# Optimization experiments

Hardware: AMD Instinct MI355X
Metric: run time of the kernel (lower is better)

## Reference

```python
import jax, jax.numpy as jnp
import numpy as np

N0, N1, N2, N3 = 100000, 200000, 150000, 50000
C = 64            # all in/intermediate/out channel widths
SLOPE = 0.2       # leaky_relu negative slope


def seg_softmax(vals, seg, n):
    """Row-wise sparse softmax (torch.sparse.softmax, dim=1) over COO values."""
    m = jax.ops.segment_max(vals, seg, num_segments=n)
    ex = jnp.exp(vals - m[seg])
    s = jax.ops.segment_sum(ex, seg, num_segments=n)
    return ex / s[seg]


def hbs(x, row, col, W, a, n):
    """HBS block (m_hop=1): att(i,j)=softmax_i(lrelu([m_i||m_j]a)); y = A_att @ m."""
    m = x @ W                                   # [n, C]
    a1, a2 = a[:C], a[C:]
    e = jax.nn.leaky_relu(m[row] @ a1 + m[col] @ a2, SLOPE)  # per-nnz logit
    att = seg_softmax(e, row, n)
    return jax.ops.segment_sum(att[:, None] * m[col], row, num_segments=n)


def hbns(xs, xt, ti, sj, Ws, Wt, a, ns, nt):
    """HBNS block. neighborhood is [nt, ns] with COO indices (ti, sj).
    Returns (message_on_source [ns,C], message_on_target [nt,C])."""
    sm = xs @ Ws                                # [ns, C] source messages
    tm = xt @ Wt                                # [nt, C] target messages
    a1, a2 = a[:C], a[C:]
    sm_j = sm[sj]
    tm_i = tm[ti]
    e = jax.nn.leaky_relu(sm_j @ a1 + tm_i @ a2, SLOPE)  # s->t logits, rows=ti
    f = jax.nn.leaky_relu(tm_i @ a1 + sm_j @ a2, SLOPE)  # t->s logits, rows=sj
    att_e = seg_softmax(e, ti, nt)
    att_f = seg_softmax(f, sj, ns)
    msg_t = jax.ops.segment_sum(att_e[:, None] * sm_j, ti, num_segments=nt)
    msg_s = jax.ops.segment_sum(att_f[:, None] * tm_i, sj, num_segments=ns)
    return msg_s, msg_t


def setup_inputs() -> dict:
    key = jax.random.key(0)
    ks = jax.random.split(key, 32)
    def randn(k, shape):
        return jax.random.normal(k, shape, dtype=jnp.float32)
    def ridx(k, n, hi):
        return jax.random.randint(k, (n,), 0, hi, dtype=jnp.int32)
    g = 0.1  # weight scale (~xavier for 64-dim)
    return dict(
        x_0=randn(ks[0], (N0, C)), x_1=randn(ks[1], (N1, C)),
        x_2=randn(ks[2], (N2, C)), x_3=randn(ks[3], (N3, C)),
        # 5 HBS blocks: [0_l1, 0_l2, 1_l2, 2_l2, 3_l2]
        hbs_W=randn(ks[4], (5, C, C)) * g,
        hbs_a=randn(ks[5], (5, 2 * C)) * g,
        # 6 HBNS blocks: [01_l1, 12_l1, 23_l1, 01_l2, 12_l2, 23_l2]
        hbns_Ws=randn(ks[6], (6, C, C)) * g,
        hbns_Wt=randn(ks[7], (6, C, C)) * g,
        hbns_a=randn(ks[8], (6, 2 * C)) * g,
        adj0_row=ridx(ks[9], 1000000, N0), adj0_col=ridx(ks[10], 1000000, N0),
        adj1_row=ridx(ks[11], 1000000, N1), adj1_col=ridx(ks[12], 1000000, N1),
        adj2_row=ridx(ks[13], 800000, N2), adj2_col=ridx(ks[14], 800000, N2),
        coadj3_row=ridx(ks[15], 300000, N3), coadj3_col=ridx(ks[16], 300000, N3),
        inc1_row=ridx(ks[17], 400000, N0), inc1_col=ridx(ks[18], 400000, N1),
        inc2_row=ridx(ks[19], 450000, N1), inc2_col=ridx(ks[20], 450000, N2),
        inc3_row=ridx(ks[21], 200000, N2), inc3_col=ridx(ks[22], 200000, N3),
    )


def reference(x_0, x_1, x_2, x_3, hbs_W, hbs_a, hbns_Ws, hbns_Wt, hbns_a,
              adj0_row, adj0_col, adj1_row, adj1_col, adj2_row, adj2_col,
              coadj3_row, coadj3_col, inc1_row, inc1_col, inc2_row, inc2_col,
              inc3_row, inc3_col):
    n0, n1, n2, n3 = x_0.shape[0], x_1.shape[0], x_2.shape[0], x_3.shape[0]
    # ---- level 1 ----
    x00 = hbs(x_0, adj0_row, adj0_col, hbs_W[0], hbs_a[0], n0)
    x01, x10 = hbns(x_1, x_0, inc1_row, inc1_col, hbns_Ws[0], hbns_Wt[0], hbns_a[0], n1, n0)
    x12, x21 = hbns(x_2, x_1, inc2_row, inc2_col, hbns_Ws[1], hbns_Wt[1], hbns_a[1], n2, n1)
    x23, x32 = hbns(x_3, x_2, inc3_row, inc3_col, hbns_Ws[2], hbns_Wt[2], hbns_a[2], n3, n2)
    x0_l1 = x00 + x10
    x1_l1 = x01 + x21
    x2_l1 = x12 + x32
    x3_l1 = x23
    # ---- level 2 ----
    y00 = hbs(x0_l1, adj0_row, adj0_col, hbs_W[1], hbs_a[1], n0)
    y11 = hbs(x1_l1, adj1_row, adj1_col, hbs_W[2], hbs_a[2], n1)
    y22 = hbs(x2_l1, adj2_row, adj2_col, hbs_W[3], hbs_a[3], n2)
    y33 = hbs(x3_l1, coadj3_row, coadj3_col, hbs_W[4], hbs_a[4], n3)
    y01, _ = hbns(x1_l1, x0_l1, inc1_row, inc1_col, hbns_Ws[3], hbns_Wt[3], hbns_a[3], n1, n0)
    y12, _ = hbns(x2_l1, x1_l1, inc2_row, inc2_col, hbns_Ws[4], hbns_Wt[4], hbns_a[4], n2, n1)
    y23, _ = hbns(x3_l1, x2_l1, inc3_row, inc3_col, hbns_Ws[5], hbns_Wt[5], hbns_a[5], n3, n2)
    return (y00, y01 + y11, y12 + y22, y23 + y33)
```

## Files before the change

kernel.cpp:

```cpp
#include <hip/hip_runtime.h>
#include <cstddef>
#include <cstdint>

#define LRELU_SLOPE 0.2f
#define SCAN_BLK 256
#define SCAN_ELEMS 2048

#define XS_STRIDE 68

__global__ __launch_bounds__(256, 4) void gemm_pq_kernel(
    const float* __restrict__ x, const float* __restrict__ W,
    const float* __restrict__ a, float* __restrict__ m,
    float* __restrict__ p, float* __restrict__ q, int n)
{
    __shared__ float xs[64 * XS_STRIDE];
    __shared__ float ws[64 * XS_STRIDE];

    const int t = threadIdx.x;
    const int rbase = blockIdx.x * 64;

    {
        const float4* __restrict__ W4 = (const float4*)W;
#pragma unroll
        for (int u = 0; u < 4; ++u) {
            int f = t + 256 * u;
            int k = f >> 4, g = f & 15;
            float4 v = W4[f];
            *(float4*)&ws[k * XS_STRIDE + 4 * g] = v;
        }
    }
    {
        const float4* __restrict__ x4 = (const float4*)x;
#pragma unroll
        for (int u = 0; u < 4; ++u) {
            int f = t + 256 * u;
            int r = f >> 4, g = f & 15;
            float4 v = make_float4(0.f, 0.f, 0.f, 0.f);
            if (rbase + r < n) v = x4[(size_t)(rbase + r) * 16 + g];
            *(float4*)&xs[r * XS_STRIDE + 4 * g] = v;
        }
    }
    __syncthreads();

    const int lane = t & 63;
    const int wv   = t >> 6;
    const int s    = lane & 15;
    const int rg   = lane >> 4;
    const int c0   = 4 * s;
    const int r0   = 16 * wv + 4 * rg;

    float acc[4][4] = {{0.f}};

#pragma unroll 2
    for (int k0 = 0; k0 < 64; k0 += 4) {
        float xr[4][4], wr[4][4];
#pragma unroll
        for (int i = 0; i < 4; ++i) {
            float4 v = *(const float4*)&xs[(r0 + i) * XS_STRIDE + k0];
            xr[i][0] = v.x; xr[i][1] = v.y; xr[i][2] = v.z; xr[i][3] = v.w;
        }
#pragma unroll
        for (int kk = 0; kk < 4; ++kk) {
            float4 v = *(const float4*)&ws[(k0 + kk) * XS_STRIDE + c0];
            wr[kk][0] = v.x; wr[kk][1] = v.y; wr[kk][2] = v.z; wr[kk][3] = v.w;
        }
#pragma unroll
        for (int kk = 0; kk < 4; ++kk)
#pragma unroll
            for (int i = 0; i < 4; ++i)
#pragma unroll
                for (int j = 0; j < 4; ++j)
                    acc[i][j] = fmaf(xr[i][kk], wr[kk][j], acc[i][j]);
    }

#pragma unroll
    for (int i = 0; i < 4; ++i) {
        int r = rbase + r0 + i;
        if (r < n)
            *(float4*)&m[(size_t)r * 64 + c0] =
                make_float4(acc[i][0], acc[i][1], acc[i][2], acc[i][3]);
    }

    const float4 a1v = *(const float4*)&a[c0];
    const float4 a2v = *(const float4*)&a[64 + c0];
    float pp[4], qq[4];
#pragma unroll
    for (int i = 0; i < 4; ++i) {
        pp[i] = fmaf(acc[i][3], a1v.w, fmaf(acc[i][2], a1v.z,
                fmaf(acc[i][1], a1v.y, acc[i][0] * a1v.x)));
        qq[i] = fmaf(acc[i][3], a2v.w, fmaf(acc[i][2], a2v.z,
                fmaf(acc[i][1], a2v.y, acc[i][0] * a2v.x)));
    }
#pragma unroll
    for (int off = 1; off < 16; off <<= 1) {
#pragma unroll
        for (int i = 0; i < 4; ++i) {
            pp[i] += __shfl_xor(pp[i], off);
            qq[i] += __shfl_xor(qq[i], off);
        }
    }
    if (s == 0) {
#pragma unroll
        for (int i = 0; i < 4; ++i) {
            int r = rbase + r0 + i;
            if (r < n) { p[r] = pp[i]; q[r] = qq[i]; }
        }
    }
}

__global__ __launch_bounds__(256) void hist1(const int* __restrict__ seg,
                                             int* __restrict__ counts, int base, int E)
{
    int k = blockIdx.x * blockDim.x + threadIdx.x;
    if (k < E) atomicAdd(&counts[base + seg[k]], 1);
}

__global__ __launch_bounds__(256) void hist2(const int* __restrict__ a, const int* __restrict__ b,
                                             int* __restrict__ counts, int baseA, int baseB, int E)
{
    int k = blockIdx.x * blockDim.x + threadIdx.x;
    if (k < E) {
        atomicAdd(&counts[baseA + a[k]], 1);
        atomicAdd(&counts[baseB + b[k]], 1);
    }
}

__global__ __launch_bounds__(SCAN_BLK) void scan_partial(const int* __restrict__ in,
                                                         int* __restrict__ out,
                                                         int* __restrict__ bsums, int n)
{
    __shared__ int lds[SCAN_BLK];
    int base = blockIdx.x * SCAN_ELEMS + threadIdx.x * 8;
    int v[8]; int s = 0;
#pragma unroll
    for (int k = 0; k < 8; ++k) { int x = (base + k < n) ? in[base + k] : 0; v[k] = s; s += x; }
    lds[threadIdx.x] = s;
    __syncthreads();
    int t = s;
    for (int off = 1; off < SCAN_BLK; off <<= 1) {
        int y = (threadIdx.x >= off) ? lds[threadIdx.x - off] : 0;
        __syncthreads();
        t += y;
        lds[threadIdx.x] = t;
        __syncthreads();
    }
    int excl = t - s;
    if (threadIdx.x == SCAN_BLK - 1) bsums[blockIdx.x] = t;
#pragma unroll
    for (int k = 0; k < 8; ++k) if (base + k < n) out[base + k] = excl + v[k];
}

__global__ __launch_bounds__(1024) void scan_top(int* __restrict__ bsums, int nb)
{
    __shared__ int lds[1024];
    int x = (threadIdx.x < nb) ? bsums[threadIdx.x] : 0;
    lds[threadIdx.x] = x;
    __syncthreads();
    int t = x;
    for (int off = 1; off < 1024; off <<= 1) {
        int y = (threadIdx.x >= off) ? lds[threadIdx.x - off] : 0;
        __syncthreads();
        t += y;
        lds[threadIdx.x] = t;
        __syncthreads();
    }
    if (threadIdx.x < nb) bsums[threadIdx.x] = t - x;
}

__global__ __launch_bounds__(256) void scan_addback(int* __restrict__ out,
                                                    const int* __restrict__ bsums, int n)
{
    int i = blockIdx.x * blockDim.x + threadIdx.x;
    if (i < n) out[i] += bsums[i / SCAN_ELEMS];
}

__global__ __launch_bounds__(256) void place1(const int* __restrict__ seg, const int* __restrict__ other,
                                              const int* __restrict__ rs, int* __restrict__ counts,
                                              int* __restrict__ colsAll, int base, int E)
{
    int k = blockIdx.x * blockDim.x + threadIdx.x;
    if (k >= E) return;
    int s = base + seg[k];
    int off = atomicSub(&counts[s], 1) - 1;
    colsAll[rs[s] + off] = other[k];
}

__global__ __launch_bounds__(256) void place2(const int* __restrict__ a, const int* __restrict__ b,
                                              const int* __restrict__ rs, int* __restrict__ counts,
                                              int* __restrict__ colsAll, int baseA, int baseB, int E)
{
    int k = blockIdx.x * blockDim.x + threadIdx.x;
    if (k >= E) return;
    int av = a[k], bv = b[k];
    int sa = baseA + av;
    int offa = atomicSub(&counts[sa], 1) - 1;
    colsAll[rs[sa] + offa] = bv;
    int sb = baseB + bv;
    int offb = atomicSub(&counts[sb], 1) - 1;
    colsAll[rs[sb] + offb] = av;
}

__global__ __launch_bounds__(256) void seg_agg(
    const int* __restrict__ rs, const int* __restrict__ cols,
    const float* __restrict__ uni, const float* __restrict__ gat,
    const float* __restrict__ feat, float* __restrict__ out, int n)
{
    const int sub = threadIdx.x & 15;
    int row = (int)((blockIdx.x * blockDim.x + threadIdx.x) >> 4);
    if (row >= n) return;
    int e0 = rs[row], e1 = rs[row + 1];
    if (e0 >= e1) return;
    const float pu = uni[row];
    const float4* __restrict__ feat4 = (const float4*)feat;
    float4 acc = make_float4(0.f, 0.f, 0.f, 0.f);
    float ssum = 0.f;
    int e = e0;
    for (; e + 1 < e1; e += 2) {
        int c0 = cols[e], c1 = cols[e + 1];
        float g0 = gat[c0], g1 = gat[c1];
        float4 f0 = feat4[(size_t)c0 * 16 + sub];
        float4 f1 = feat4[(size_t)c1 * 16 + sub];
        float t0 = pu + g0; t0 = (t0 > 0.f) ? t0 : LRELU_SLOPE * t0;
        float t1 = pu + g1; t1 = (t1 > 0.f) ? t1 : LRELU_SLOPE * t1;
        float w0 = __expf(t0);
        float w1 = __expf(t1);
        ssum += w0 + w1;
        acc.x = fmaf(w0, f0.x, acc.x); acc.y = fmaf(w0, f0.y, acc.y);
        acc.z = fmaf(w0, f0.z, acc.z); acc.w = fmaf(w0, f0.w, acc.w);
        acc.x = fmaf(w1, f1.x, acc.x); acc.y = fmaf(w1, f1.y, acc.y);
        acc.z = fmaf(w1, f1.z, acc.z); acc.w = fmaf(w1, f1.w, acc.w);
    }
    if (e < e1) {
        int c0 = cols[e];
        float g0 = gat[c0];
        float4 f0 = feat4[(size_t)c0 * 16 + sub];
        float t0 = pu + g0; t0 = (t0 > 0.f) ? t0 : LRELU_SLOPE * t0;
        float w0 = __expf(t0);
        ssum += w0;
        acc.x = fmaf(w0, f0.x, acc.x); acc.y = fmaf(w0, f0.y, acc.y);
        acc.z = fmaf(w0, f0.z, acc.z); acc.w = fmaf(w0, f0.w, acc.w);
    }
    float inv = __frcp_rn(ssum);
    float4* __restrict__ out4 = (float4*)out;
    float4 o = out4[(size_t)row * 16 + sub];
    o.x = fmaf(acc.x, inv, o.x); o.y = fmaf(acc.y, inv, o.y);
    o.z = fmaf(acc.z, inv, o.z); o.w = fmaf(acc.w, inv, o.w);
    out4[(size_t)row * 16 + sub] = o;
}

extern "C" void kernel_launch(void* const* d_in, const int* in_sizes, int n_in,
                              void* d_out, int out_size, void* d_ws, size_t ws_size,
                              hipStream_t stream)
{
    const float* x0 = (const float*)d_in[0];
    const float* x1 = (const float*)d_in[1];
    const float* x2 = (const float*)d_in[2];
    const float* x3 = (const float*)d_in[3];
    const float* hbsW = (const float*)d_in[4];
    const float* hbsA = (const float*)d_in[5];
    const float* hWs  = (const float*)d_in[6];
    const float* hWt  = (const float*)d_in[7];
    const float* hA   = (const float*)d_in[8];
    const int* a0r = (const int*)d_in[9];  const int* a0c = (const int*)d_in[10];
    const int* a1r = (const int*)d_in[11]; const int* a1c = (const int*)d_in[12];
    const int* a2r = (const int*)d_in[13]; const int* a2c = (const int*)d_in[14];
    const int* c3r = (const int*)d_in[15]; const int* c3c = (const int*)d_in[16];
    const int* i1r = (const int*)d_in[17]; const int* i1c = (const int*)d_in[18];
    const int* i2r = (const int*)d_in[19]; const int* i2c = (const int*)d_in[20];
    const int* i3r = (const int*)d_in[21]; const int* i3c = (const int*)d_in[22];

    const int n0 = in_sizes[0] / 64, n1 = in_sizes[1] / 64;
    const int n2 = in_sizes[2] / 64, n3 = in_sizes[3] / 64;
    const int Ea0 = in_sizes[9],  Ea1 = in_sizes[11], Ea2 = in_sizes[13], Ec3 = in_sizes[15];
    const int Ei1 = in_sizes[17], Ei2 = in_sizes[19], Ei3 = in_sizes[21];

    int nm = n0; if (n1 > nm) nm = n1; if (n2 > nm) nm = n2; if (n3 > nm) nm = n3;

    int b_adj0 = 0;
    int b_adj1 = b_adj0 + n0;
    int b_adj2 = b_adj1 + n1;
    int b_c3   = b_adj2 + n2;
    int b_i1t  = b_c3   + n3;
    int b_i1s  = b_i1t  + n0;
    int b_i2t  = b_i1s  + n1;
    int b_i2s  = b_i2t  + n1;
    int b_i3t  = b_i2s  + n2;
    int b_i3s  = b_i3t  + n2;
    int NC     = b_i3s  + n3 + 1;
    long long eTot = (long long)Ea0 + Ea1 + Ea2 + Ec3 + 2LL * (Ei1 + Ei2 + Ei3);

    float* w = (float*)d_ws;
    size_t off = 0;
    auto allocf = [&](size_t nel) { float* r = w + off; off += nel; return r; };
    float* featA = allocf((size_t)nm * 64);
    float* featB = allocf((size_t)nm * 64);
    float* xl10  = allocf((size_t)n0 * 64);
    float* xl11  = allocf((size_t)n1 * 64);
    float* xl12  = allocf((size_t)n2 * 64);
    float* xl13  = allocf((size_t)n3 * 64);
    float* pA = allocf(nm); float* qA = allocf(nm);
    float* pB = allocf(nm); float* qB = allocf(nm);
    int* counts  = (int*)allocf((size_t)NC);
    int* rs      = (int*)allocf((size_t)NC);
    int* bsums   = (int*)allocf(1024);
    int* colsAll = (int*)allocf((size_t)eTot);

    if (off * sizeof(float) > ws_size) {
        hipMemsetAsync(d_out, 0, (size_t)out_size * sizeof(float), stream);
        return;
    }

    float* out  = (float*)d_out;
    float* out0 = out;
    float* out1 = out0 + (size_t)n0 * 64;
    float* out2 = out1 + (size_t)n1 * 64;
    float* out3 = out2 + (size_t)n2 * 64;

    hipMemsetAsync(xl10, 0, (size_t)(n0 + n1 + n2 + n3) * 64 * sizeof(float), stream);
    hipMemsetAsync(counts, 0, (size_t)NC * sizeof(int), stream);
    hipMemsetAsync(d_out, 0, (size_t)out_size * sizeof(float), stream);

    auto blks = [](int n, int per) { return dim3((unsigned)((n + per - 1) / per)); };

    hist1<<<blks(Ea0, 256), 256, 0, stream>>>(a0r, counts, b_adj0, Ea0);
    hist1<<<blks(Ea1, 256), 256, 0, stream>>>(a1r, counts, b_adj1, Ea1);
    hist1<<<blks(Ea2, 256), 256, 0, stream>>>(a2r, counts, b_adj2, Ea2);
    hist1<<<blks(Ec3, 256), 256, 0, stream>>>(c3r, counts, b_c3,  Ec3);
    hist2<<<blks(Ei1, 256), 256, 0, stream>>>(i1r, i1c, counts, b_i1t, b_i1s, Ei1);
    hist2<<<blks(Ei2, 256), 256, 0, stream>>>(i2r, i2c, counts, b_i2t, b_i2s, Ei2);
    hist2<<<blks(Ei3, 256), 256, 0, stream>>>(i3r, i3c, counts, b_i3t, b_i3s, Ei3);

    int nb = (NC + SCAN_ELEMS - 1) / SCAN_ELEMS;
    scan_partial<<<dim3((unsigned)nb), SCAN_BLK, 0, stream>>>(counts, rs, bsums, NC);
    scan_top<<<dim3(1), 1024, 0, stream>>>(bsums, nb);
    scan_addback<<<blks(NC, 256), 256, 0, stream>>>(rs, bsums, NC);

    place1<<<blks(Ea0, 256), 256, 0, stream>>>(a0r, a0c, rs, counts, colsAll, b_adj0, Ea0);
    place1<<<blks(Ea1, 256), 256, 0, stream>>>(a1r, a1c, rs, counts, colsAll, b_adj1, Ea1);
    place1<<<blks(Ea2, 256), 256, 0, stream>>>(a2r, a2c, rs, counts, colsAll, b_adj2, Ea2);
    place1<<<blks(Ec3, 256), 256, 0, stream>>>(c3r, c3c, rs, counts, colsAll, b_c3,  Ec3);
    place2<<<blks(Ei1, 256), 256, 0, stream>>>(i1r, i1c, rs, counts, colsAll, b_i1t, b_i1s, Ei1);
    place2<<<blks(Ei2, 256), 256, 0, stream>>>(i2r, i2c, rs, counts, colsAll, b_i2t, b_i2s, Ei2);
    place2<<<blks(Ei3, 256), 256, 0, stream>>>(i3r, i3c, rs, counts, colsAll, b_i3t, b_i3s, Ei3);

    auto gemm = [&](const float* xx, const float* WW, const float* aa,
                    float* mm, float* pp, float* qq, int n) {
        gemm_pq_kernel<<<blks(n, 64), 256, 0, stream>>>(xx, WW, aa, mm, pp, qq, n);
    };
    auto agg = [&](int base, const float* uni, const float* gat,
                   const float* feat, float* outp, int n) {
        seg_agg<<<blks(n, 16), 256, 0, stream>>>(rs + base, colsAll, uni, gat, feat, outp, n);
    };

    gemm(x0, hbsW + 0 * 4096, hbsA + 0 * 128, featA, pA, qA, n0);
    agg(b_adj0, pA, qA, featA, xl10, n0);

    gemm(x1, hWs + 0 * 4096, hA + 0 * 128, featA, pA, qA, n1);
    gemm(x0, hWt + 0 * 4096, hA + 0 * 128, featB, pB, qB, n0);
    agg(b_i1t, qB, pA, featA, xl10, n0);
    agg(b_i1s, qA, pB, featB, xl11, n1);

    gemm(x2, hWs + 1 * 4096, hA + 1 * 128, featA, pA, qA, n2);
    gemm(x1, hWt + 1 * 4096, hA + 1 * 128, featB, pB, qB, n1);
    agg(b_i2t, qB, pA, featA, xl11, n1);
    agg(b_i2s, qA, pB, featB, xl12, n2);

    gemm(x3, hWs + 2 * 4096, hA + 2 * 128, featA, pA, qA, n3);
    gemm(x2, hWt + 2 * 4096, hA + 2 * 128, featB, pB, qB, n2);
    agg(b_i3t, qB, pA, featA, xl12, n2);
    agg(b_i3s, qA, pB, featB, xl13, n3);

    gemm(xl10, hbsW + 1 * 4096, hbsA + 1 * 128, featA, pA, qA, n0);
    agg(b_adj0, pA, qA, featA, out0, n0);

    gemm(xl11, hbsW + 2 * 4096, hbsA + 2 * 128, featA, pA, qA, n1);
    agg(b_adj1, pA, qA, featA, out1, n1);

    gemm(xl12, hbsW + 3 * 4096, hbsA + 3 * 128, featA, pA, qA, n2);
    agg(b_adj2, pA, qA, featA, out2, n2);

    gemm(xl13, hbsW + 4 * 4096, hbsA + 4 * 128, featA, pA, qA, n3);
    agg(b_c3, pA, qA, featA, out3, n3);

    gemm(xl11, hWs + 3 * 4096, hA + 3 * 128, featA, pA, qA, n1);
    gemm(xl10, hWt + 3 * 4096, hA + 3 * 128, featB, pB, qB, n0);
    agg(b_i1s, qA, pB, featB, out1, n1);

    gemm(xl12, hWs + 4 * 4096, hA + 4 * 128, featA, pA, qA, n2);
    gemm(xl11, hWt + 4 * 4096, hA + 4 * 128, featB, pB, qB, n1);
    agg(b_i2s, qA, pB, featB, out2, n2);

    gemm(xl13, hWs + 5 * 4096, hA + 5 * 128, featA, pA, qA, n3);
    gemm(xl12, hWs != hWt ? hWt + 5 * 4096 : hWt + 5 * 4096, hA + 5 * 128, featB, pB, qB, n2);
    agg(b_i3s, qA, pB, featB, out3, n3);
}
```

Measured before the change: 1.727 ms.

## Drop output memsets via store-mode aggregation and vectorize COO histogram/placement

Adds a STORE template mode to seg_agg so the first aggregation into each buffer writes its result directly, zero-filling empty rows, instead of read-modify-writing a pre-zeroed buffer. This removes two large memsets and a read per row on first writes. The histogram and placement kernels now have each thread handle four edges through int4 loads, with the grid shrunk to match. The gain depends on every output buffer being written first by a STORE call, so a wrong call order would silently corrupt results.

```diff
diff --git a/kernel.cpp b/kernel.cpp
--- a/kernel.cpp
+++ b/kernel.cpp
@@ -111,17 +111,38 @@
 __global__ __launch_bounds__(256) void hist1(const int* __restrict__ seg,
                                              int* __restrict__ counts, int base, int E)
 {
-    int k = blockIdx.x * blockDim.x + threadIdx.x;
-    if (k < E) atomicAdd(&counts[base + seg[k]], 1);
+    int k0 = (blockIdx.x * blockDim.x + threadIdx.x) * 4;
+    if (k0 + 3 < E) {
+        int4 s4 = *(const int4*)&seg[k0];
+        atomicAdd(&counts[base + s4.x], 1);
+        atomicAdd(&counts[base + s4.y], 1);
+        atomicAdd(&counts[base + s4.z], 1);
+        atomicAdd(&counts[base + s4.w], 1);
+    } else {
+        for (int k = k0; k < E; ++k) atomicAdd(&counts[base + seg[k]], 1);
+    }
 }
 
 __global__ __launch_bounds__(256) void hist2(const int* __restrict__ a, const int* __restrict__ b,
                                              int* __restrict__ counts, int baseA, int baseB, int E)
 {
-    int k = blockIdx.x * blockDim.x + threadIdx.x;
-    if (k < E) {
-        atomicAdd(&counts[baseA + a[k]], 1);
-        atomicAdd(&counts[baseB + b[k]], 1);
+    int k0 = (blockIdx.x * blockDim.x + threadIdx.x) * 4;
+    if (k0 + 3 < E) {
+        int4 a4 = *(const int4*)&a[k0];
+        int4 b4 = *(const int4*)&b[k0];
+        atomicAdd(&counts[baseA + a4.x], 1);
+        atomicAdd(&counts[baseA + a4.y], 1);
+        atomicAdd(&counts[baseA + a4.z], 1);
+        atomicAdd(&counts[baseA + a4.w], 1);
+        atomicAdd(&counts[baseB + b4.x], 1);
+        atomicAdd(&counts[baseB + b4.y], 1);
+        atomicAdd(&counts[baseB + b4.z], 1);
+        atomicAdd(&counts[baseB + b4.w], 1);
+    } else {
+        for (int k = k0; k < E; ++k) {
+            atomicAdd(&counts[baseA + a[k]], 1);
+            atomicAdd(&counts[baseB + b[k]], 1);
+        }
     }
 }
 
@@ -178,28 +199,68 @@
                                               const int* __restrict__ rs, int* __restrict__ counts,
                                               int* __restrict__ colsAll, int base, int E)
 {
-    int k = blockIdx.x * blockDim.x + threadIdx.x;
-    if (k >= E) return;
-    int s = base + seg[k];
-    int off = atomicSub(&counts[s], 1) - 1;
-    colsAll[rs[s] + off] = other[k];
+    int k0 = (blockIdx.x * blockDim.x + threadIdx.x) * 4;
+    if (k0 + 3 < E) {
+        int4 s4 = *(const int4*)&seg[k0];
+        int4 o4 = *(const int4*)&other[k0];
+        int sa = base + s4.x, sb = base + s4.y, sc = base + s4.z, sd = base + s4.w;
+        int oa = atomicSub(&counts[sa], 1) - 1;
+        int ob = atomicSub(&counts[sb], 1) - 1;
+        int oc = atomicSub(&counts[sc], 1) - 1;
+        int od = atomicSub(&counts[sd], 1) - 1;
+        colsAll[rs[sa] + oa] = o4.x;
+        colsAll[rs[sb] + ob] = o4.y;
+        colsAll[rs[sc] + oc] = o4.z;
+        colsAll[rs[sd] + od] = o4.w;
+    } else {
+        for (int k = k0; k < E; ++k) {
+            int s = base + seg[k];
+            int off = atomicSub(&counts[s], 1) - 1;
+            colsAll[rs[s] + off] = other[k];
+        }
+    }
 }
 
 __global__ __launch_bounds__(256) void place2(const int* __restrict__ a, const int* __restrict__ b,
                                               const int* __restrict__ rs, int* __restrict__ counts,
                                               int* __restrict__ colsAll, int baseA, int baseB, int E)
 {
-    int k = blockIdx.x * blockDim.x + threadIdx.x;
-    if (k >= E) return;
-    int av = a[k], bv = b[k];
-    int sa = baseA + av;
-    int offa = atomicSub(&counts[sa], 1) - 1;
-    colsAll[rs[sa] + offa] = bv;
-    int sb = baseB + bv;
-    int offb = atomicSub(&counts[sb], 1) - 1;
-    colsAll[rs[sb] + offb] = av;
-}
-
+    int k0 = (blockIdx.x * blockDim.x + threadIdx.x) * 4;
+    if (k0 + 3 < E) {
+        int4 a4 = *(const int4*)&a[k0];
+        int4 b4 = *(const int4*)&b[k0];
+        int sa0 = baseA + a4.x, sa1 = baseA + a4.y, sa2 = baseA + a4.z, sa3 = baseA + a4.w;
+        int sb0 = baseB + b4.x, sb1 = baseB + b4.y, sb2 = baseB + b4.z, sb3 = baseB + b4.w;
+        int oa0 = atomicSub(&counts[sa0], 1) - 1;
+        int oa1 = atomicSub(&counts[sa1], 1) - 1;
+        int oa2 = atomicSub(&counts[sa2], 1) - 1;
+        int oa3 = atomicSub(&counts[sa3], 1) - 1;
+        int ob0 = atomicSub(&counts[sb0], 1) - 1;
+        int ob1 = atomicSub(&counts[sb1], 1) - 1;
+        int ob2 = atomicSub(&counts[sb2], 1) - 1;
+        int ob3 = atomicSub(&counts[sb3], 1) - 1;
+        colsAll[rs[sa0] + oa0] = b4.x;
+        colsAll[rs[sa1] + oa1] = b4.y;
+        colsAll[rs[sa2] + oa2] = b4.z;
+        colsAll[rs[sa3] + oa3] = b4.w;
+        colsAll[rs[sb0] + ob0] = a4.x;
+        colsAll[rs[sb1] + ob1] = a4.y;
+        colsAll[rs[sb2] + ob2] = a4.z;
+        colsAll[rs[sb3] + ob3] = a4.w;
+    } else {
+        for (int k = k0; k < E; ++k) {
+            int av = a[k], bv = b[k];
+            int sa = baseA + av;
+            int offa = atomicSub(&counts[sa], 1) - 1;
+            colsAll[rs[sa] + offa] = bv;
+            int sb = baseB + bv;
+            int offb = atomicSub(&counts[sb], 1) - 1;
+            colsAll[rs[sb] + offb] = av;
+        }
+    }
+}
+
+template<bool STORE>
 __global__ __launch_bounds__(256) void seg_agg(
     const int* __restrict__ rs, const int* __restrict__ cols,
     const float* __restrict__ uni, const float* __restrict__ gat,
@@ -208,8 +269,12 @@
     const int sub = threadIdx.x & 15;
     int row = (int)((blockIdx.x * blockDim.x + threadIdx.x) >> 4);
     if (row >= n) return;
+    float4* __restrict__ out4 = (float4*)out;
     int e0 = rs[row], e1 = rs[row + 1];
-    if (e0 >= e1) return;
+    if (e0 >= e1) {
+        if (STORE) out4[(size_t)row * 16 + sub] = make_float4(0.f, 0.f, 0.f, 0.f);
+        return;
+    }
     const float pu = uni[row];
     const float4* __restrict__ feat4 = (const float4*)feat;
     float4 acc = make_float4(0.f, 0.f, 0.f, 0.f);
@@ -241,11 +306,15 @@
         acc.z = fmaf(w0, f0.z, acc.z); acc.w = fmaf(w0, f0.w, acc.w);
     }
     float inv = __frcp_rn(ssum);
-    float4* __restrict__ out4 = (float4*)out;
-    float4 o = out4[(size_t)row * 16 + sub];
-    o.x = fmaf(acc.x, inv, o.x); o.y = fmaf(acc.y, inv, o.y);
-    o.z = fmaf(acc.z, inv, o.z); o.w = fmaf(acc.w, inv, o.w);
-    out4[(size_t)row * 16 + sub] = o;
+    if (STORE) {
+        out4[(size_t)row * 16 + sub] =
+            make_float4(acc.x * inv, acc.y * inv, acc.z * inv, acc.w * inv);
+    } else {
+        float4 o = out4[(size_t)row * 16 + sub];
+        o.x = fmaf(acc.x, inv, o.x); o.y = fmaf(acc.y, inv, o.y);
+        o.z = fmaf(acc.z, inv, o.z); o.w = fmaf(acc.w, inv, o.w);
+        out4[(size_t)row * 16 + sub] = o;
+    }
 }
 
 extern "C" void kernel_launch(void* const* d_in, const int* in_sizes, int n_in,
@@ -316,81 +385,83 @@
     float* out2 = out1 + (size_t)n1 * 64;
     float* out3 = out2 + (size_t)n2 * 64;
 
-    hipMemsetAsync(xl10, 0, (size_t)(n0 + n1 + n2 + n3) * 64 * sizeof(float), stream);
     hipMemsetAsync(counts, 0, (size_t)NC * sizeof(int), stream);
-    hipMemsetAsync(d_out, 0, (size_t)out_size * sizeof(float), stream);
 
     auto blks = [](int n, int per) { return dim3((unsigned)((n + per - 1) / per)); };
 
-    hist1<<<blks(Ea0, 256), 256, 0, stream>>>(a0r, counts, b_adj0, Ea0);
-    hist1<<<blks(Ea1, 256), 256, 0, stream>>>(a1r, counts, b_adj1, Ea1);
-    hist1<<<blks(Ea2, 256), 256, 0, stream>>>(a2r, counts, b_adj2, Ea2);
-    hist1<<<blks(Ec3, 256), 256, 0, stream>>>(c3r, counts, b_c3,  Ec3);
-    hist2<<<blks(Ei1, 256), 256, 0, stream>>>(i1r, i1c, counts, b_i1t, b_i1s, Ei1);
-    hist2<<<blks(Ei2, 256), 256, 0, stream>>>(i2r, i2c, counts, b_i2t, b_i2s, Ei2);
-    hist2<<<blks(Ei3, 256), 256, 0, stream>>>(i3r, i3c, counts, b_i3t, b_i3s, Ei3);
+    hist1<<<blks(Ea0, 1024), 256, 0, stream>>>(a0r, counts, b_adj0, Ea0);
+    hist1<<<blks(Ea1, 1024), 256, 0, stream>>>(a1r, counts, b_adj1, Ea1);
+    hist1<<<blks(Ea2, 1024), 256, 0, stream>>>(a2r, counts, b_adj2, Ea2);
+    hist1<<<blks(Ec3, 1024), 256, 0, stream>>>(c3r, counts, b_c3,  Ec3);
+    hist2<<<blks(Ei1, 1024), 256, 0, stream>>>(i1r, i1c, counts, b_i1t, b_i1s, Ei1);
+    hist2<<<blks(Ei2, 1024), 256, 0, stream>>>(i2r, i2c, counts, b_i2t, b_i2s, Ei2);
+    hist2<<<blks(Ei3, 1024), 256, 0, stream>>>(i3r, i3c, counts, b_i3t, b_i3s, Ei3);
 
     int nb = (NC + SCAN_ELEMS - 1) / SCAN_ELEMS;
     scan_partial<<<dim3((unsigned)nb), SCAN_BLK, 0, stream>>>(counts, rs, bsums, NC);
     scan_top<<<dim3(1), 1024, 0, stream>>>(bsums, nb);
     scan_addback<<<blks(NC, 256), 256, 0, stream>>>(rs, bsums, NC);
 
-    place1<<<blks(Ea0, 256), 256, 0, stream>>>(a0r, a0c, rs, counts, colsAll, b_adj0, Ea0);
-    place1<<<blks(Ea1, 256), 256, 0, stream>>>(a1r, a1c, rs, counts, colsAll, b_adj1, Ea1);
-    place1<<<blks(Ea2, 256), 256, 0, stream>>>(a2r, a2c, rs, counts, colsAll, b_adj2, Ea2);
-    place1<<<blks(Ec3, 256), 256, 0, stream>>>(c3r, c3c, rs, counts, colsAll, b_c3,  Ec3);
-    place2<<<blks(Ei1, 256), 256, 0, stream>>>(i1r, i1c, rs, counts, colsAll, b_i1t, b_i1s, Ei1);
-    place2<<<blks(Ei2, 256), 256, 0, stream>>>(i2r, i2c, rs, counts, colsAll, b_i2t, b_i2s, Ei2);
-    place2<<<blks(Ei3, 256), 256, 0, stream>>>(i3r, i3c, rs, counts, colsAll, b_i3t, b_i3s, Ei3);
+    place1<<<blks(Ea0, 1024), 256, 0, stream>>>(a0r, a0c, rs, counts, colsAll, b_adj0, Ea0);
+    place1<<<blks(Ea1, 1024), 256, 0, stream>>>(a1r, a1c, rs, counts, colsAll, b_adj1, Ea1);
+    place1<<<blks(Ea2, 1024), 256, 0, stream>>>(a2r, a2c, rs, counts, colsAll, b_adj2, Ea2);
+    place1<<<blks(Ec3, 1024), 256, 0, stream>>>(c3r, c3c, rs, counts, colsAll, b_c3,  Ec3);
+    place2<<<blks(Ei1, 1024), 256, 0, stream>>>(i1r, i1c, rs, counts, colsAll, b_i1t, b_i1s, Ei1);
+    place2<<<blks(Ei2, 1024), 256, 0, stream>>>(i2r, i2c, rs, counts, colsAll, b_i2t, b_i2s, Ei2);
+    place2<<<blks(Ei3, 1024), 256, 0, stream>>>(i3r, i3c, rs, counts, colsAll, b_i3t, b_i3s, Ei3);
 
     auto gemm = [&](const float* xx, const float* WW, const float* aa,
                     float* mm, float* pp, float* qq, int n) {
         gemm_pq_kernel<<<blks(n, 64), 256, 0, stream>>>(xx, WW, aa, mm, pp, qq, n);
     };
-    auto agg = [&](int base, const float* uni, const float* gat,
-                   const float* feat, float* outp, int n) {
-        seg_agg<<<blks(n, 16), 256, 0, stream>>>(rs + base, colsAll, uni, gat, feat, outp, n);
+    auto aggS = [&](int base, const float* uni, const float* gat,
+                    const float* feat, float* outp, int n) {
+        seg_agg<true><<<blks(n, 16), 256, 0, stream>>>(rs + base, colsAll, uni, gat, feat, outp, n);
     };
+    auto aggA = [&](int base, const float* uni, const float* gat,
+                    const float* feat, float* outp, int n) {
+        seg_agg<false><<<blks(n, 16), 256, 0, stream>>>(rs + base, colsAll, uni, gat, feat, outp, n);
+    };
 
     gemm(x0, hbsW + 0 * 4096, hbsA + 0 * 128, featA, pA, qA, n0);
-    agg(b_adj0, pA, qA, featA, xl10, n0);
+    aggS(b_adj0, pA, qA, featA, xl10, n0);
 
     gemm(x1, hWs + 0 * 4096, hA + 0 * 128, featA, pA, qA, n1);
     gemm(x0, hWt + 0 * 4096, hA + 0 * 128, featB, pB, qB, n0);
-    agg(b_i1t, qB, pA, featA, xl10, n0);
-    agg(b_i1s, qA, pB, featB, xl11, n1);
+    aggA(b_i1t, qB, pA, featA, xl10, n0);
+    aggS(b_i1s, qA, pB, featB, xl11, n1);
 
     gemm(x2, hWs + 1 * 4096, hA + 1 * 128, featA, pA, qA, n2);
     gemm(x1, hWt + 1 * 4096, hA + 1 * 128, featB, pB, qB, n1);
-    agg(b_i2t, qB, pA, featA, xl11, n1);
-    agg(b_i2s, qA, pB, featB, xl12, n2);
+    aggA(b_i2t, qB, pA, featA, xl11, n1);
+    aggS(b_i2s, qA, pB, featB, xl12, n2);
 
     gemm(x3, hWs + 2 * 4096, hA + 2 * 128, featA, pA, qA, n3);
     gemm(x2, hWt + 2 * 4096, hA + 2 * 128, featB, pB, qB, n2);
-    agg(b_i3t, qB, pA, featA, xl12, n2);
-    agg(b_i3s, qA, pB, featB, xl13, n3);
+    aggA(b_i3t, qB, pA, featA, xl12, n2);
+    aggS(b_i3s, qA, pB, featB, xl13, n3);
 
     gemm(xl10, hbsW + 1 * 4096, hbsA + 1 * 128, featA, pA, qA, n0);
-    agg(b_adj0, pA, qA, featA, out0, n0);
+    aggS(b_adj0, pA, qA, featA, out0, n0);
 
     gemm(xl11, hbsW + 2 * 4096, hbsA + 2 * 128, featA, pA, qA, n1);
-    agg(b_adj1, pA, qA, featA, out1, n1);
+    aggS(b_adj1, pA, qA, featA, out1, n1);
 
     gemm(xl12, hbsW + 3 * 4096, hbsA + 3 * 128, featA, pA, qA, n2);
-    agg(b_adj2, pA, qA, featA, out2, n2);
+    aggS(b_adj2, pA, qA, featA, out2, n2);
 
     gemm(xl13, hbsW + 4 * 4096, hbsA + 4 * 128, featA, pA, qA, n3);
-    agg(b_c3, pA, qA, featA, out3, n3);
+    aggS(b_c3, pA, qA, featA, out3, n3);
 
     gemm(xl11, hWs + 3 * 4096, hA + 3 * 128, featA, pA, qA, n1);
     gemm(xl10, hWt + 3 * 4096, hA + 3 * 128, featB, pB, qB, n0);
-    agg(b_i1s, qA, pB, featB, out1, n1);
+    aggA(b_i1s, qA, pB, featB, out1, n1);
 
     gemm(xl12, hWs + 4 * 4096, hA + 4 * 128, featA, pA, qA, n2);
     gemm(xl11, hWt + 4 * 4096, hA + 4 * 128, featB, pB, qB, n1);
-    agg(b_i2s, qA, pB, featB, out2, n2);
+    aggA(b_i2s, qA, pB, featB, out2, n2);
 
     gemm(xl13, hWs + 5 * 4096, hA + 5 * 128, featA, pA, qA, n3);
-    gemm(xl12, hWs != hWt ? hWt + 5 * 4096 : hWt + 5 * 4096, hA + 5 * 128, featB, pB, qB, n2);
-    agg(b_i3s, qA, pB, featB, out3, n3);
-}
+    gemm(xl12, hWt + 5 * 4096, hA + 5 * 128, featB, pB, qB, n2);
+    aggA(b_i3s, qA, pB, featB, out3, n3);
+}
```

After: 1.660 ms. 1.04x faster.
